# Kernel tuning notes

Measured on AMD Instinct MI355X. Metric: run time of the kernel, lower is better.

The kernel has to match this reference:

```python
import jax, jax.numpy as jnp
import numpy as np

EPS = 1e-5

def _lin_bn_relu(x, W, b, gamma, beta):
    # x: [N, Cin], W: [Cout, Cin] (torch layout), b/gamma/beta: [Cout]
    y = x @ W.T + b
    mu = jnp.mean(y, axis=0)                      # training-mode batch stats
    var = jnp.mean((y - mu) ** 2, axis=0)         # biased variance (torch BN)
    yhat = (y - mu) * jax.lax.rsqrt(var + EPS)
    return jax.nn.relu(gamma * yhat + beta)


def setup_inputs() -> dict:
    key = jax.random.key(0)
    ks = jax.random.split(key, 16)
    N = 262144
    dims = [(64, 3), (512, 64), (512, 512), (2, 512)]
    inp = {
        "x1": jax.random.normal(ks[0], (8, 4, 8, 8), dtype=jnp.float32),
        "x2": jax.random.normal(ks[1], (N, 3), dtype=jnp.float32),
    }
    for i, (co, ci) in enumerate(dims, start=1):
        lim = 1.0 / np.sqrt(ci)
        inp[f"W{i}"] = jax.random.uniform(ks[2 * i], (co, ci), jnp.float32, -lim, lim)
        inp[f"b{i}"] = jax.random.uniform(ks[2 * i + 1], (co,), jnp.float32, -lim, lim)
    for i, c in enumerate([64, 512, 512], start=1):
        inp[f"gamma{i}"] = jnp.ones((c,), jnp.float32)
        inp[f"beta{i}"] = jnp.zeros((c,), jnp.float32)
    return inp


def reference(x1, x2, W1, b1, W2, b2, W3, b3, W4, b4,
              gamma1, beta1, gamma2, beta2, gamma3, beta3):
    # x1 is sliced in the original forward (x[0][:, 0:-1]) but unused in the output.
    h = _lin_bn_relu(x2, W1, b1, gamma1, beta1)   # [N, 64]
    h = _lin_bn_relu(h, W2, b2, gamma2, beta2)    # [N, 512]
    h = _lin_bn_relu(h, W3, b3, gamma3, beta3)    # [N, 512]
    out = h @ W4.T + b4                           # [N, 2]
    return out
```

## Files before the change

kernel.cpp:

```cpp
#include <hip/hip_runtime.h>

typedef __bf16 bf16x4 __attribute__((ext_vector_type(4)));
typedef __bf16 bf16x8 __attribute__((ext_vector_type(8)));
typedef float f32x4 __attribute__((ext_vector_type(4)));

#define MFMA_BF16 __builtin_amdgcn_mfma_f32_16x16x32_bf16

__global__ __launch_bounds__(256) void prep_stats1_kernel(
    const float* __restrict__ x, const float* __restrict__ W1,
    const float* __restrict__ b1, const float* __restrict__ W2,
    const float* __restrict__ W3, __bf16* __restrict__ W2bf,
    __bf16* __restrict__ W3bf, float* __restrict__ gsum,
    float* __restrict__ gsq) {
  const int b = blockIdx.x;
  const int t = threadIdx.x;
  if (b >= 2048) {
    const float* src;
    __bf16* dst;
    int idx;
    if (b < 2064) {
      idx = (b - 2048) * 2048 + t * 8;
      src = W2;
      dst = W2bf;
    } else {
      idx = (b - 2064) * 2048 + t * 8;
      src = W3;
      dst = W3bf;
    }
    float4 f0 = *(const float4*)(src + idx);
    float4 f1 = *(const float4*)(src + idx + 4);
    bf16x8 o;
    o[0] = (__bf16)f0.x;
    o[1] = (__bf16)f0.y;
    o[2] = (__bf16)f0.z;
    o[3] = (__bf16)f0.w;
    o[4] = (__bf16)f1.x;
    o[5] = (__bf16)f1.y;
    o[6] = (__bf16)f1.z;
    o[7] = (__bf16)f1.w;
    *(bf16x8*)(dst + idx) = o;
    return;
  }
  int c = t & 63;
  int rw = t >> 6;
  float w0 = W1[c * 3 + 0], w1 = W1[c * 3 + 1], w2 = W1[c * 3 + 2];
  float bb = b1[c];
  int base = b * 128;
  float sum = 0.f, sq = 0.f;
#pragma unroll 4
  for (int i = 0; i < 32; ++i) {
    int row = base + i * 4 + rw;
    const float* xp = x + (size_t)row * 3;
    float y = fmaf(xp[0], w0, fmaf(xp[1], w1, fmaf(xp[2], w2, bb)));
    sum += y;
    sq += y * y;
  }
  __shared__ float ssum[256], ssq[256];
  ssum[t] = sum;
  ssq[t] = sq;
  __syncthreads();
  if (t < 64) {
    float s = ssum[t] + ssum[t + 64] + ssum[t + 128] + ssum[t + 192];
    float q = ssq[t] + ssq[t + 64] + ssq[t + 128] + ssq[t + 192];
    atomicAdd(&gsum[t], s);
    atomicAdd(&gsq[t], q);
  }
}

__global__ __launch_bounds__(256, 4) void m1_kernel(
    const float* __restrict__ x2, const float* __restrict__ gsum1,
    const float* __restrict__ gsq1, const float* __restrict__ gamma1,
    const float* __restrict__ beta1, const float* __restrict__ W1,
    const float* __restrict__ b1, float* __restrict__ M1,
    float* __restrict__ s1, float invN) {
  __shared__ float sF[256];
  __shared__ float xs[768];
  __shared__ __bf16 h1T[64 * 264];
  __shared__ float s1s[4][64];

  const int t = threadIdx.x;
  const int lane = t & 63, wave = t >> 6;
  const int lrow = lane & 15, lgrp = lane >> 4;

  if (t < 64) {
    float mu = gsum1[t] * invN;
    float var = gsq1[t] * invN - mu * mu;
    float sc = gamma1[t] * rsqrtf(var + 1e-5f);
    float sh = beta1[t] - mu * sc;
    sF[t] = sc * W1[t * 3];
    sF[64 + t] = sc * W1[t * 3 + 1];
    sF[128 + t] = sc * W1[t * 3 + 2];
    sF[192 + t] = sc * b1[t] + sh;
  }
  if (t < 192)
    ((float4*)xs)[t] = ((const float4*)(x2 + (size_t)blockIdx.x * 768))[t];
  __syncthreads();

  const int c0 = (t & 3) * 16;
  const int r0 = t >> 2;
  float sAcc[16] = {};
#pragma unroll
  for (int s = 0; s < 4; ++s) {
    int r = r0 + s * 64;
    float X0 = xs[r * 3], X1 = xs[r * 3 + 1], X2 = xs[r * 3 + 2];
#pragma unroll
    for (int j = 0; j < 16; ++j) {
      int c = c0 + j;
      float h = fmaxf(
          fmaf(sF[c], X0, fmaf(sF[64 + c], X1, fmaf(sF[128 + c], X2, sF[192 + c]))),
          0.f);
      sAcc[j] += h;
      h1T[c * 264 + r] = (__bf16)h;
    }
  }
  __syncthreads();

  f32x4 acc[4] = {};
#pragma unroll
  for (int kk = 0; kk < 256; kk += 32) {
    bf16x8 af = *(const bf16x8*)&h1T[(wave * 16 + lrow) * 264 + kk + lgrp * 8];
#pragma unroll
    for (int n = 0; n < 4; ++n) {
      bf16x8 bfr = *(const bf16x8*)&h1T[(n * 16 + lrow) * 264 + kk + lgrp * 8];
      acc[n] = MFMA_BF16(af, bfr, acc[n], 0, 0, 0);
    }
  }
#pragma unroll
  for (int n = 0; n < 4; ++n)
#pragma unroll
    for (int rr = 0; rr < 4; ++rr)
      atomicAdd(&M1[(wave * 16 + lgrp * 4 + rr) * 64 + n * 16 + lrow],
                acc[n][rr]);

#pragma unroll
  for (int j = 0; j < 16; ++j) {
    float v = sAcc[j];
    v += __shfl_xor(v, 4);
    v += __shfl_xor(v, 8);
    v += __shfl_xor(v, 16);
    v += __shfl_xor(v, 32);
    if (lane < 4) s1s[wave][(lane & 3) * 16 + j] = v;
  }
  __syncthreads();
  if (t < 64)
    atomicAdd(&s1[t], s1s[0][t] + s1s[1][t] + s1s[2][t] + s1s[3][t]);
}

__global__ __launch_bounds__(256) void finalize2v_kernel(
    const float* __restrict__ M1, const float* __restrict__ s1,
    const float* __restrict__ W2, const float* __restrict__ b2,
    const float* __restrict__ gamma2, const float* __restrict__ beta2,
    float* __restrict__ scale2, float* __restrict__ shift2f, float fN) {
  __shared__ float sM[64 * 65];
  __shared__ float ss[64];
  int t = threadIdx.x;
  for (int i = t; i < 4096; i += 256) sM[(i >> 6) * 65 + (i & 63)] = M1[i];
  if (t < 64) ss[t] = s1[t];
  __syncthreads();
  int lane = t & 63;
  int col = blockIdx.x * 4 + (t >> 6);
  float wi = W2[(size_t)col * 64 + lane];
  float p = 0.f;
#pragma unroll
  for (int j = 0; j < 64; ++j) p = fmaf(sM[lane * 65 + j], __shfl(wi, j), p);
  float qi = wi * p;
  float swi = ss[lane] * wi;
#pragma unroll
  for (int off = 1; off < 64; off <<= 1) {
    qi += __shfl_xor(qi, off);
    swi += __shfl_xor(swi, off);
  }
  if (lane == 0) {
    float b = b2[col];
    float sy = swi + fN * b;
    float sqs = qi + 2.f * b * swi + fN * b * b;
    float mu = sy / fN;
    float var = sqs / fN - mu * mu;
    float sc = gamma2[col] * rsqrtf(var + 1e-5f);
    scale2[col] = sc;
    shift2f[col] = (beta2[col] - mu * sc) + sc * b;
  }
}

#define G3_LD(BUF, K)                                                        \
  _Pragma("unroll") for (int m = 0; m < 4; ++m) BUF[m] =                     \
      *(const bf16x8*)&h2r[(m * 16 + lrow) * 520 + (K) * 32 + lgrp * 8];

#define G3_MM(BUF, K)                                                        \
  __builtin_amdgcn_s_setprio(1);                                             \
  _Pragma("unroll") for (int m = 0; m < 4; ++m) {                            \
    acc[m][0] = MFMA_BF16(BUF[m], b3r[K][0], acc[m][0], 0, 0, 0);            \
    acc[m][1] = MFMA_BF16(BUF[m], b3r[K][1], acc[m][1], 0, 0, 0);            \
  }                                                                          \
  __builtin_amdgcn_s_setprio(0);

template <int MODE>
__global__ __launch_bounds__(512, 2) void fused_kernel(
    const float* __restrict__ x2, const float* __restrict__ gsum1,
    const float* __restrict__ gsq1, const float* __restrict__ gamma1,
    const float* __restrict__ beta1, const float* __restrict__ W1,
    const float* __restrict__ b1, const __bf16* __restrict__ W2bf,
    const float* __restrict__ scale2, const float* __restrict__ shift2f,
    const __bf16* __restrict__ W3bf, const float* __restrict__ b3,
    const float* __restrict__ gamma3, const float* __restrict__ beta3,
    const float* __restrict__ W4, const float* __restrict__ b4,
    float* __restrict__ gsum3, float* __restrict__ gsq3,
    float* __restrict__ out, __bf16* __restrict__ y3o, int gBase, int gCount,
    int rStoreRgs, float invN) {
  __shared__ __bf16 h1buf[2][64 * 72];
  __shared__ __bf16 h2buf[2][64 * 520];
  __shared__ float sF[256];
  __shared__ float sSc2[512], sSh2[512];
  __shared__ float outaccW[8][64][2];

  const int t = threadIdx.x;
  const int lane = t & 63, wave = t >> 6;
  const int lrow = lane & 15, lgrp = lane >> 4;
  const int colHalf = blockIdx.x & 1;
  const int rgFirst = gBase + (int)(blockIdx.x >> 1) * gCount;
  const int wCol3 = colHalf * 256 + wave * 32;
  const int wCol2 = wave * 64;
  const bool doStore = (MODE == 3) && (rgFirst < rStoreRgs);

  if (t < 64) {
    float mu = gsum1[t] * invN;
    float var = gsq1[t] * invN - mu * mu;
    float sc = gamma1[t] * rsqrtf(var + 1e-5f);
    float sh = beta1[t] - mu * sc;
    sF[t] = sc * W1[t * 3];
    sF[64 + t] = sc * W1[t * 3 + 1];
    sF[128 + t] = sc * W1[t * 3 + 2];
    sF[192 + t] = sc * b1[t] + sh;
  }
  sSc2[t] = scale2[t & 511];
  sSh2[t] = shift2f[t & 511];

  bf16x8 b2r[2][4];
#pragma unroll
  for (int kk = 0; kk < 2; ++kk)
#pragma unroll
    for (int n = 0; n < 4; ++n)
      b2r[kk][n] = *(const bf16x8*)&W2bf[(wCol2 + n * 16 + lrow) * 64 +
                                         kk * 32 + lgrp * 8];
  bf16x8 b3r[16][2];
#pragma unroll
  for (int k = 0; k < 16; ++k)
#pragma unroll
    for (int n = 0; n < 2; ++n)
      b3r[k][n] = *(const bf16x8*)&W3bf[(size_t)(wCol3 + n * 16 + lrow) * 512 +
                                        k * 32 + lgrp * 8];

  const int c3a = wCol3 + lrow, c3b = wCol3 + 16 + lrow;
  float b3a = 0.f, b3b = 0.f;
  float sc3a = 0.f, sc3b = 0.f, sh3a = 0.f, sh3b = 0.f;
  float w40a = 0.f, w40b = 0.f, w41a = 0.f, w41b = 0.f, B40 = 0.f, B41 = 0.f;
  if (MODE != 2) {
    b3a = b3[c3a];
    b3b = b3[c3b];
  } else {
    float mu = gsum3[c3a] * invN;
    float var = gsq3[c3a] * invN - mu * mu;
    sc3a = gamma3[c3a] * rsqrtf(var + 1e-5f);
    sh3a = sc3a * b3[c3a] + (beta3[c3a] - mu * sc3a);
    mu = gsum3[c3b] * invN;
    var = gsq3[c3b] * invN - mu * mu;
    sc3b = gamma3[c3b] * rsqrtf(var + 1e-5f);
    sh3b = sc3b * b3[c3b] + (beta3[c3b] - mu * sc3b);
    w40a = W4[c3a];
    w40b = W4[c3b];
    w41a = W4[512 + c3a];
    w41b = W4[512 + c3b];
    B40 = b4[0];
    B41 = b4[1];
  }
  float csA = 0.f, cqA = 0.f, csB = 0.f, cqB = 0.f;

  const int hr = t >> 3, hc0 = (t & 7) * 8;
  const float* xbase = x2 + ((size_t)rgFirst * 64 + hr) * 3;
  float xa, xb, xc;

  auto stageH1 = [&](__bf16* h1p) {
    bf16x8 hv;
#pragma unroll
    for (int j = 0; j < 8; ++j) {
      int c = hc0 + j;
      float h = fmaf(sF[c], xa,
                     fmaf(sF[64 + c], xb, fmaf(sF[128 + c], xc, sF[192 + c])));
      hv[j] = (__bf16)fmaxf(h, 0.f);
    }
    *(bf16x8*)&h1p[hr * 72 + hc0] = hv;
  };

  auto gemm2 = [&](const __bf16* h1p, __bf16* h2p) {
#pragma unroll
    for (int nh = 0; nh < 2; ++nh) {
      f32x4 a2[2][4] = {};
#pragma unroll
      for (int kk = 0; kk < 2; ++kk) {
        bf16x8 af0 = *(const bf16x8*)&h1p[(0 * 16 + lrow) * 72 + kk * 32 + lgrp * 8];
        bf16x8 af1 = *(const bf16x8*)&h1p[(1 * 16 + lrow) * 72 + kk * 32 + lgrp * 8];
        bf16x8 af2 = *(const bf16x8*)&h1p[(2 * 16 + lrow) * 72 + kk * 32 + lgrp * 8];
        bf16x8 af3 = *(const bf16x8*)&h1p[(3 * 16 + lrow) * 72 + kk * 32 + lgrp * 8];
#pragma unroll
        for (int n2 = 0; n2 < 2; ++n2) {
          int n = nh * 2 + n2;
          a2[n2][0] = MFMA_BF16(b2r[kk][n], af0, a2[n2][0], 0, 0, 0);
          a2[n2][1] = MFMA_BF16(b2r[kk][n], af1, a2[n2][1], 0, 0, 0);
          a2[n2][2] = MFMA_BF16(b2r[kk][n], af2, a2[n2][2], 0, 0, 0);
          a2[n2][3] = MFMA_BF16(b2r[kk][n], af3, a2[n2][3], 0, 0, 0);
        }
      }
#pragma unroll
      for (int n2 = 0; n2 < 2; ++n2) {
        int ch0 = wCol2 + (nh * 2 + n2) * 16 + lgrp * 4;
        float s0 = sSc2[ch0], s1v = sSc2[ch0 + 1], s2v = sSc2[ch0 + 2],
              s3v = sSc2[ch0 + 3];
        float z0 = sSh2[ch0], z1 = sSh2[ch0 + 1], z2 = sSh2[ch0 + 2],
              z3 = sSh2[ch0 + 3];
#pragma unroll
        for (int m = 0; m < 4; ++m) {
          int row = m * 16 + lrow;
          bf16x4 hv;
          hv[0] = (__bf16)fmaxf(fmaf(s0, a2[n2][m][0], z0), 0.f);
          hv[1] = (__bf16)fmaxf(fmaf(s1v, a2[n2][m][1], z1), 0.f);
          hv[2] = (__bf16)fmaxf(fmaf(s2v, a2[n2][m][2], z2), 0.f);
          hv[3] = (__bf16)fmaxf(fmaf(s3v, a2[n2][m][3], z3), 0.f);
          *(bf16x4*)&h2p[row * 520 + ch0] = hv;
        }
      }
    }
  };

  __syncthreads();

  xa = xbase[0];
  xb = xbase[1];
  xc = xbase[2];
  stageH1(h1buf[0]);
  __syncthreads();
  gemm2(h1buf[0], h2buf[0]);
  if (gCount > 1) {
    const float* xn = xbase + 192;
    xa = xn[0];
    xb = xn[1];
    xc = xn[2];
    stageH1(h1buf[1]);
  }
  __syncthreads();

  for (int g = 0; g < gCount; ++g) {
    const int rBase = (rgFirst + g) * 64;
    const __bf16* h2r = h2buf[g & 1];

    if (g + 2 < gCount) {
      const float* xn = xbase + (size_t)(g + 2) * 192;
      xa = xn[0];
      xb = xn[1];
      xc = xn[2];
    }

    if (g + 1 < gCount) gemm2(h1buf[(g + 1) & 1], h2buf[(g + 1) & 1]);
    if (g + 2 < gCount) stageH1(h1buf[g & 1]);

    f32x4 acc[4][2] = {};
    bf16x8 afA[4], afB[4];
    G3_LD(afA, 0)
#pragma unroll
    for (int k = 0; k < 16; k += 2) {
      G3_LD(afB, k + 1)
      G3_MM(afA, k)
      if (k < 14) { G3_LD(afA, k + 2) }
      G3_MM(afB, k + 1)
    }

    if (MODE != 2) {
#pragma unroll
      for (int m = 0; m < 4; ++m)
#pragma unroll
        for (int rr = 0; rr < 4; ++rr) {
          float ya = acc[m][0][rr] + b3a;
          float yb = acc[m][1][rr] + b3b;
          csA += ya;
          cqA = fmaf(ya, ya, cqA);
          csB += yb;
          cqB = fmaf(yb, yb, cqB);
          if (doStore) {
            size_t row = (size_t)(rBase + m * 16 + lgrp * 4 + rr);
            y3o[row * 512 + c3a] = (__bf16)ya;
            y3o[row * 512 + c3b] = (__bf16)yb;
          }
        }
    } else {
#pragma unroll
      for (int m = 0; m < 4; ++m)
#pragma unroll
        for (int rr = 0; rr < 4; ++rr) {
          float ha = fmaxf(fmaf(sc3a, acc[m][0][rr], sh3a), 0.f);
          float hb = fmaxf(fmaf(sc3b, acc[m][1][rr], sh3b), 0.f);
          float dd0 = fmaf(ha, w40a, hb * w40b);
          float dd1 = fmaf(ha, w41a, hb * w41b);
          dd0 += __shfl_xor(dd0, 1);
          dd1 += __shfl_xor(dd1, 1);
          dd0 += __shfl_xor(dd0, 2);
          dd1 += __shfl_xor(dd1, 2);
          dd0 += __shfl_xor(dd0, 4);
          dd1 += __shfl_xor(dd1, 4);
          dd0 += __shfl_xor(dd0, 8);
          dd1 += __shfl_xor(dd1, 8);
          if (lrow == 0) {
            int row = m * 16 + lgrp * 4 + rr;
            outaccW[wave][row][0] = dd0;
            outaccW[wave][row][1] = dd1;
          }
        }
    }
    __syncthreads();
  }

  if (MODE != 2) {
    csA += __shfl_xor(csA, 16);
    cqA += __shfl_xor(cqA, 16);
    csB += __shfl_xor(csB, 16);
    cqB += __shfl_xor(cqB, 16);
    csA += __shfl_xor(csA, 32);
    cqA += __shfl_xor(cqA, 32);
    csB += __shfl_xor(csB, 32);
    cqB += __shfl_xor(cqB, 32);
    if (lgrp == 0) {
      atomicAdd(&gsum3[c3a], csA);
      atomicAdd(&gsq3[c3a], cqA);
      atomicAdd(&gsum3[c3b], csB);
      atomicAdd(&gsq3[c3b], cqB);
    }
  } else {
    if (t < 128) {
      int row = t >> 1, o = t & 1;
      float s = 0.f;
#pragma unroll
      for (int w = 0; w < 8; ++w) s += outaccW[w][row][o];
      if (colHalf == 0) s += (o == 0) ? B40 : B41;
      atomicAdd(&out[(size_t)(rgFirst * 64 + row) * 2 + o], s);
    }
  }
}

__global__ __launch_bounds__(256) void stream_out_kernel(
    const __bf16* __restrict__ y3, const float* __restrict__ gsum3,
    const float* __restrict__ gsq3, const float* __restrict__ gamma3,
    const float* __restrict__ beta3, const float* __restrict__ W4,
    const float* __restrict__ b4, float* __restrict__ out, int N, float invN) {
  __shared__ float sSc[512], sSh[512], sW0[512], sW1[512];
  int t = threadIdx.x;
  for (int i = t; i < 512; i += 256) {
    float mu = gsum3[i] * invN;
    float var = gsq3[i] * invN - mu * mu;
    float sc = gamma3[i] * rsqrtf(var + 1e-5f);
    sSc[i] = sc;
    sSh[i] = beta3[i] - mu * sc;
    sW0[i] = W4[i];
    sW1[i] = W4[512 + i];
  }
  __syncthreads();
  int lane = t & 63, wv = t >> 6;
  int c0 = lane * 8;
  float fsc[8], fsh[8], fw0[8], fw1[8];
#pragma unroll
  for (int j = 0; j < 8; ++j) {
    fsc[j] = sSc[c0 + j];
    fsh[j] = sSh[c0 + j];
    fw0[j] = sW0[c0 + j];
    fw1[j] = sW1[c0 + j];
  }
  float B0 = b4[0], B1 = b4[1];
  for (size_t row = (size_t)blockIdx.x * 8 + wv * 2; row < (size_t)N;
       row += (size_t)gridDim.x * 8) {
    bf16x8 v0 = *(const bf16x8*)(y3 + row * 512 + c0);
    bf16x8 v1 = *(const bf16x8*)(y3 + (row + 1) * 512 + c0);
    float d0a = 0.f, d1a = 0.f, d0b = 0.f, d1b = 0.f;
#pragma unroll
    for (int j = 0; j < 8; ++j) {
      float ha = fmaxf(fmaf(fsc[j], (float)v0[j], fsh[j]), 0.f);
      float hb = fmaxf(fmaf(fsc[j], (float)v1[j], fsh[j]), 0.f);
      d0a = fmaf(ha, fw0[j], d0a);
      d1a = fmaf(ha, fw1[j], d1a);
      d0b = fmaf(hb, fw0[j], d0b);
      d1b = fmaf(hb, fw1[j], d1b);
    }
    float t0 = d0a + __shfl_xor(d0a, 1);
    float t1 = d1a + __shfl_xor(d1a, 1);
    float t2 = d0b + __shfl_xor(d0b, 1);
    float t3 = d1b + __shfl_xor(d1b, 1);
    float u0 = (lane & 1) ? t1 : t0;
    float u1 = (lane & 1) ? t3 : t2;
    u0 += __shfl_xor(u0, 2);
    u1 += __shfl_xor(u1, 2);
    float w = (lane & 2) ? u1 : u0;
    w += __shfl_xor(w, 4);
    w += __shfl_xor(w, 8);
    w += __shfl_xor(w, 16);
    w += __shfl_xor(w, 32);
    if (lane < 4) out[row * 2 + lane] = w + ((lane & 1) ? B1 : B0);
  }
}

extern "C" void kernel_launch(void* const* d_in, const int* in_sizes, int n_in,
                              void* d_out, int out_size, void* d_ws,
                              size_t ws_size, hipStream_t stream) {
  const float* x2 = (const float*)d_in[1];
  const float* W1 = (const float*)d_in[2];
  const float* b1 = (const float*)d_in[3];
  const float* W2 = (const float*)d_in[4];
  const float* b2 = (const float*)d_in[5];
  const float* W3 = (const float*)d_in[6];
  const float* b3 = (const float*)d_in[7];
  const float* W4 = (const float*)d_in[8];
  const float* b4 = (const float*)d_in[9];
  const float* gamma1 = (const float*)d_in[10];
  const float* beta1 = (const float*)d_in[11];
  const float* gamma2 = (const float*)d_in[12];
  const float* beta2 = (const float*)d_in[13];
  const float* gamma3 = (const float*)d_in[14];
  const float* beta3 = (const float*)d_in[15];
  float* out = (float*)d_out;

  const int N = in_sizes[1] / 3;
  const float invN = 1.0f / (float)N;

  float* f0 = (float*)d_ws;
  float* gsum1 = f0;
  float* gsq1 = f0 + 64;
  float* M1 = f0 + 128;
  float* s1 = f0 + 4224;
  float* gsum3 = f0 + 4288;
  float* gsq3 = f0 + 4800;
  float* scale2 = f0 + 5312;
  float* shift2f = f0 + 5824;
  __bf16* W2bf = (__bf16*)(f0 + 6336);
  __bf16* W3bf = W2bf + 32768;

  const size_t y3off = (size_t)1 << 20;
  size_t availRows = (ws_size > y3off) ? (ws_size - y3off) / 1024 : 0;
  int rStoreBlks = (int)((availRows / 1024 < (size_t)(N / 1024))
                             ? availRows / 1024
                             : (size_t)(N / 1024));
  const int rStore = rStoreBlks * 1024;
  __bf16* y3bf = (__bf16*)((char*)d_ws + y3off);

  hipMemsetAsync(f0, 0, 5312 * sizeof(float), stream);
  prep_stats1_kernel<<<2192, 256, 0, stream>>>(x2, W1, b1, W2, W3, W2bf, W3bf,
                                               gsum1, gsq1);
  m1_kernel<<<N / 256, 256, 0, stream>>>(x2, gsum1, gsq1, gamma1, beta1, W1,
                                         b1, M1, s1, invN);
  finalize2v_kernel<<<128, 256, 0, stream>>>(M1, s1, W2, b2, gamma2, beta2,
                                             scale2, shift2f, (float)N);

  fused_kernel<3><<<(N / 1024) * 2, 512, 0, stream>>>(
      x2, gsum1, gsq1, gamma1, beta1, W1, b1, W2bf, scale2, shift2f, W3bf, b3,
      gamma3, beta3, W4, b4, gsum3, gsq3, out, y3bf, 0, 16, rStoreBlks * 16,
      invN);

  if (rStore > 0)
    stream_out_kernel<<<2048, 256, 0, stream>>>(y3bf, gsum3, gsq3, gamma3,
                                                beta3, W4, b4, out, rStore,
                                                invN);
  if (rStore < N) {
    hipMemsetAsync(out + (size_t)rStore * 2, 0,
                   (size_t)(N - rStore) * 2 * sizeof(float), stream);
    fused_kernel<2><<<((N - rStore) / 64) * 2, 512, 0, stream>>>(
        x2, gsum1, gsq1, gamma1, beta1, W1, b1, W2bf, scale2, shift2f, W3bf,
        b3, gamma3, beta3, W4, b4, gsum3, gsq3, out, y3bf, rStore / 64, 1, 0,
        invN);
  }
}
```

Before: 384.1 us.

## Derive BN1 stats from input moments; stagger gemm2/gemm3 order across waves

Replaces the per-channel layer-1 sum and sum-of-squares pass with a reduction of the nine first- and second-order moments of the 3-wide input. BN1 mean and variance are then computed analytically from W1 and b1 inside each consumer kernel. This cuts the stats kernel from 2048 blocks to 64 and reduces global atomics to 9 per block. Separately, in the fused kernel, half the waves run gemm3 before gemm2/stageH1 while the other half run it after, so MFMA and LDS phases interleave across waves. The moment formula in fp32 over 262k rows may lose some precision in the variance.

New measurement: 403.1 us. 1.05x slower.

```diff
diff --git a/kernel.cpp b/kernel.cpp
--- a/kernel.cpp
+++ b/kernel.cpp
@@ -6,24 +6,22 @@
 
 #define MFMA_BF16 __builtin_amdgcn_mfma_f32_16x16x32_bf16
 
-__global__ __launch_bounds__(256) void prep_stats1_kernel(
-    const float* __restrict__ x, const float* __restrict__ W1,
-    const float* __restrict__ b1, const float* __restrict__ W2,
+__global__ __launch_bounds__(256) void prep_xmom_kernel(
+    const float* __restrict__ x, const float* __restrict__ W2,
     const float* __restrict__ W3, __bf16* __restrict__ W2bf,
-    __bf16* __restrict__ W3bf, float* __restrict__ gsum,
-    float* __restrict__ gsq) {
+    __bf16* __restrict__ W3bf, float* __restrict__ xmom) {
   const int b = blockIdx.x;
   const int t = threadIdx.x;
-  if (b >= 2048) {
+  if (b >= 64) {
     const float* src;
     __bf16* dst;
     int idx;
-    if (b < 2064) {
-      idx = (b - 2048) * 2048 + t * 8;
+    if (b < 80) {
+      idx = (b - 64) * 2048 + t * 8;
       src = W2;
       dst = W2bf;
     } else {
-      idx = (b - 2064) * 2048 + t * 8;
+      idx = (b - 80) * 2048 + t * 8;
       src = W3;
       dst = W3bf;
     }
@@ -41,38 +39,68 @@
     *(bf16x8*)(dst + idx) = o;
     return;
   }
-  int c = t & 63;
-  int rw = t >> 6;
-  float w0 = W1[c * 3 + 0], w1 = W1[c * 3 + 1], w2 = W1[c * 3 + 2];
-  float bb = b1[c];
-  int base = b * 128;
-  float sum = 0.f, sq = 0.f;
+  float m[9] = {};
 #pragma unroll 4
-  for (int i = 0; i < 32; ++i) {
-    int row = base + i * 4 + rw;
-    const float* xp = x + (size_t)row * 3;
-    float y = fmaf(xp[0], w0, fmaf(xp[1], w1, fmaf(xp[2], w2, bb)));
-    sum += y;
-    sq += y * y;
-  }
-  __shared__ float ssum[256], ssq[256];
-  ssum[t] = sum;
-  ssq[t] = sq;
-  __syncthreads();
-  if (t < 64) {
-    float s = ssum[t] + ssum[t + 64] + ssum[t + 128] + ssum[t + 192];
-    float q = ssq[t] + ssq[t + 64] + ssq[t + 128] + ssq[t + 192];
-    atomicAdd(&gsum[t], s);
-    atomicAdd(&gsq[t], q);
-  }
+  for (int i = 0; i < 16; ++i) {
+    int r = b * 4096 + i * 256 + t;
+    const float* xp = x + (size_t)r * 3;
+    float a = xp[0], bb = xp[1], c = xp[2];
+    m[0] += a;
+    m[1] += bb;
+    m[2] += c;
+    m[3] = fmaf(a, a, m[3]);
+    m[4] = fmaf(a, bb, m[4]);
+    m[5] = fmaf(a, c, m[5]);
+    m[6] = fmaf(bb, bb, m[6]);
+    m[7] = fmaf(bb, c, m[7]);
+    m[8] = fmaf(c, c, m[8]);
+  }
+  __shared__ float red[4][9];
+  int lane = t & 63, wave = t >> 6;
+#pragma unroll
+  for (int j = 0; j < 9; ++j) {
+    float v = m[j];
+    v += __shfl_xor(v, 1);
+    v += __shfl_xor(v, 2);
+    v += __shfl_xor(v, 4);
+    v += __shfl_xor(v, 8);
+    v += __shfl_xor(v, 16);
+    v += __shfl_xor(v, 32);
+    if (lane == 0) red[wave][j] = v;
+  }
+  __syncthreads();
+  if (t < 9) atomicAdd(&xmom[t], red[0][t] + red[1][t] + red[2][t] + red[3][t]);
 }
 
+__device__ __forceinline__ void bn1_fold(const float* __restrict__ xm,
+                                         const float* __restrict__ W1,
+                                         const float* __restrict__ b1,
+                                         const float* __restrict__ gamma1,
+                                         const float* __restrict__ beta1,
+                                         int c, float invN, float fN,
+                                         float* f0, float* f1, float* f2,
+                                         float* f3) {
+  float w0 = W1[c * 3], w1 = W1[c * 3 + 1], w2 = W1[c * 3 + 2], bb = b1[c];
+  float wx = w0 * xm[0] + w1 * xm[1] + w2 * xm[2];
+  float sy = wx + fN * bb;
+  float q = w0 * w0 * xm[3] + 2.f * w0 * w1 * xm[4] + 2.f * w0 * w2 * xm[5] +
+            w1 * w1 * xm[6] + 2.f * w1 * w2 * xm[7] + w2 * w2 * xm[8] +
+            2.f * bb * wx + fN * bb * bb;
+  float mu = sy * invN;
+  float var = q * invN - mu * mu;
+  float sc = gamma1[c] * rsqrtf(var + 1e-5f);
+  float sh = beta1[c] - mu * sc;
+  *f0 = sc * w0;
+  *f1 = sc * w1;
+  *f2 = sc * w2;
+  *f3 = sc * bb + sh;
+}
+
 __global__ __launch_bounds__(256, 4) void m1_kernel(
-    const float* __restrict__ x2, const float* __restrict__ gsum1,
-    const float* __restrict__ gsq1, const float* __restrict__ gamma1,
-    const float* __restrict__ beta1, const float* __restrict__ W1,
-    const float* __restrict__ b1, float* __restrict__ M1,
-    float* __restrict__ s1, float invN) {
+    const float* __restrict__ x2, const float* __restrict__ xmom,
+    const float* __restrict__ gamma1, const float* __restrict__ beta1,
+    const float* __restrict__ W1, const float* __restrict__ b1,
+    float* __restrict__ M1, float* __restrict__ s1, float invN, float fN) {
   __shared__ float sF[256];
   __shared__ float xs[768];
   __shared__ __bf16 h1T[64 * 264];
@@ -83,14 +111,12 @@
   const int lrow = lane & 15, lgrp = lane >> 4;
 
   if (t < 64) {
-    float mu = gsum1[t] * invN;
-    float var = gsq1[t] * invN - mu * mu;
-    float sc = gamma1[t] * rsqrtf(var + 1e-5f);
-    float sh = beta1[t] - mu * sc;
-    sF[t] = sc * W1[t * 3];
-    sF[64 + t] = sc * W1[t * 3 + 1];
-    sF[128 + t] = sc * W1[t * 3 + 2];
-    sF[192 + t] = sc * b1[t] + sh;
+    float f0, f1, f2, f3;
+    bn1_fold(xmom, W1, b1, gamma1, beta1, t, invN, fN, &f0, &f1, &f2, &f3);
+    sF[t] = f0;
+    sF[64 + t] = f1;
+    sF[128 + t] = f2;
+    sF[192 + t] = f3;
   }
   if (t < 192)
     ((float4*)xs)[t] = ((const float4*)(x2 + (size_t)blockIdx.x * 768))[t];
@@ -196,17 +222,17 @@
 
 template <int MODE>
 __global__ __launch_bounds__(512, 2) void fused_kernel(
-    const float* __restrict__ x2, const float* __restrict__ gsum1,
-    const float* __restrict__ gsq1, const float* __restrict__ gamma1,
-    const float* __restrict__ beta1, const float* __restrict__ W1,
-    const float* __restrict__ b1, const __bf16* __restrict__ W2bf,
-    const float* __restrict__ scale2, const float* __restrict__ shift2f,
-    const __bf16* __restrict__ W3bf, const float* __restrict__ b3,
-    const float* __restrict__ gamma3, const float* __restrict__ beta3,
-    const float* __restrict__ W4, const float* __restrict__ b4,
-    float* __restrict__ gsum3, float* __restrict__ gsq3,
-    float* __restrict__ out, __bf16* __restrict__ y3o, int gBase, int gCount,
-    int rStoreRgs, float invN) {
+    const float* __restrict__ x2, const float* __restrict__ xmom,
+    const float* __restrict__ gamma1, const float* __restrict__ beta1,
+    const float* __restrict__ W1, const float* __restrict__ b1,
+    const __bf16* __restrict__ W2bf, const float* __restrict__ scale2,
+    const float* __restrict__ shift2f, const __bf16* __restrict__ W3bf,
+    const float* __restrict__ b3, const float* __restrict__ gamma3,
+    const float* __restrict__ beta3, const float* __restrict__ W4,
+    const float* __restrict__ b4, float* __restrict__ gsum3,
+    float* __restrict__ gsq3, float* __restrict__ out,
+    __bf16* __restrict__ y3o, int gBase, int gCount, int rStoreRgs,
+    float invN, float fN) {
   __shared__ __bf16 h1buf[2][64 * 72];
   __shared__ __bf16 h2buf[2][64 * 520];
   __shared__ float sF[256];
@@ -223,14 +249,12 @@
   const bool doStore = (MODE == 3) && (rgFirst < rStoreRgs);
 
   if (t < 64) {
-    float mu = gsum1[t] * invN;
-    float var = gsq1[t] * invN - mu * mu;
-    float sc = gamma1[t] * rsqrtf(var + 1e-5f);
-    float sh = beta1[t] - mu * sc;
-    sF[t] = sc * W1[t * 3];
-    sF[64 + t] = sc * W1[t * 3 + 1];
-    sF[128 + t] = sc * W1[t * 3 + 2];
-    sF[192 + t] = sc * b1[t] + sh;
+    float f0, f1, f2, f3;
+    bn1_fold(xmom, W1, b1, gamma1, beta1, t, invN, fN, &f0, &f1, &f2, &f3);
+    sF[t] = f0;
+    sF[64 + t] = f1;
+    sF[128 + t] = f2;
+    sF[192 + t] = f3;
   }
   sSc2[t] = scale2[t & 511];
   sSh2[t] = shift2f[t & 511];
@@ -359,18 +383,31 @@
       xc = xn[2];
     }
 
-    if (g + 1 < gCount) gemm2(h1buf[(g + 1) & 1], h2buf[(g + 1) & 1]);
-    if (g + 2 < gCount) stageH1(h1buf[g & 1]);
-
-    f32x4 acc[4][2] = {};
-    bf16x8 afA[4], afB[4];
-    G3_LD(afA, 0)
-#pragma unroll
-    for (int k = 0; k < 16; k += 2) {
-      G3_LD(afB, k + 1)
-      G3_MM(afA, k)
-      if (k < 14) { G3_LD(afA, k + 2) }
-      G3_MM(afB, k + 1)
+    f32x4 acc[4][2];
+    auto gemm3 = [&]() {
+#pragma unroll
+      for (int m = 0; m < 4; ++m)
+#pragma unroll
+        for (int n = 0; n < 2; ++n) acc[m][n] = (f32x4){0.f, 0.f, 0.f, 0.f};
+      bf16x8 afA[4], afB[4];
+      G3_LD(afA, 0)
+#pragma unroll
+      for (int k = 0; k < 16; k += 2) {
+        G3_LD(afB, k + 1)
+        G3_MM(afA, k)
+        if (k < 14) { G3_LD(afA, k + 2) }
+        G3_MM(afB, k + 1)
+      }
+    };
+
+    if (wave < 4) {
+      if (g + 1 < gCount) gemm2(h1buf[(g + 1) & 1], h2buf[(g + 1) & 1]);
+      if (g + 2 < gCount) stageH1(h1buf[g & 1]);
+      gemm3();
+    } else {
+      gemm3();
+      if (g + 1 < gCount) gemm2(h1buf[(g + 1) & 1], h2buf[(g + 1) & 1]);
+      if (g + 2 < gCount) stageH1(h1buf[g & 1]);
     }
 
     if (MODE != 2) {
@@ -525,17 +562,17 @@
 
   const int N = in_sizes[1] / 3;
   const float invN = 1.0f / (float)N;
+  const float fN = (float)N;
 
   float* f0 = (float*)d_ws;
-  float* gsum1 = f0;
-  float* gsq1 = f0 + 64;
-  float* M1 = f0 + 128;
-  float* s1 = f0 + 4224;
-  float* gsum3 = f0 + 4288;
-  float* gsq3 = f0 + 4800;
-  float* scale2 = f0 + 5312;
-  float* shift2f = f0 + 5824;
-  __bf16* W2bf = (__bf16*)(f0 + 6336);
+  float* xmom = f0;
+  float* M1 = f0 + 16;
+  float* s1 = f0 + 4112;
+  float* gsum3 = f0 + 4176;
+  float* gsq3 = f0 + 4688;
+  float* scale2 = f0 + 5200;
+  float* shift2f = f0 + 5712;
+  __bf16* W2bf = (__bf16*)(f0 + 6224);
   __bf16* W3bf = W2bf + 32768;
 
   const size_t y3off = (size_t)1 << 20;
@@ -546,18 +583,17 @@
   const int rStore = rStoreBlks * 1024;
   __bf16* y3bf = (__bf16*)((char*)d_ws + y3off);
 
-  hipMemsetAsync(f0, 0, 5312 * sizeof(float), stream);
-  prep_stats1_kernel<<<2192, 256, 0, stream>>>(x2, W1, b1, W2, W3, W2bf, W3bf,
-                                               gsum1, gsq1);
-  m1_kernel<<<N / 256, 256, 0, stream>>>(x2, gsum1, gsq1, gamma1, beta1, W1,
-                                         b1, M1, s1, invN);
+  hipMemsetAsync(f0, 0, 5200 * sizeof(float), stream);
+  prep_xmom_kernel<<<208, 256, 0, stream>>>(x2, W2, W3, W2bf, W3bf, xmom);
+  m1_kernel<<<N / 256, 256, 0, stream>>>(x2, xmom, gamma1, beta1, W1, b1, M1,
+                                         s1, invN, fN);
   finalize2v_kernel<<<128, 256, 0, stream>>>(M1, s1, W2, b2, gamma2, beta2,
-                                             scale2, shift2f, (float)N);
+                                             scale2, shift2f, fN);
 
   fused_kernel<3><<<(N / 1024) * 2, 512, 0, stream>>>(
-      x2, gsum1, gsq1, gamma1, beta1, W1, b1, W2bf, scale2, shift2f, W3bf, b3,
+      x2, xmom, gamma1, beta1, W1, b1, W2bf, scale2, shift2f, W3bf, b3,
       gamma3, beta3, W4, b4, gsum3, gsq3, out, y3bf, 0, 16, rStoreBlks * 16,
-      invN);
+      invN, fN);
 
   if (rStore > 0)
     stream_out_kernel<<<2048, 256, 0, stream>>>(y3bf, gsum3, gsq3, gamma3,
@@ -567,8 +603,8 @@
     hipMemsetAsync(out + (size_t)rStore * 2, 0,
                    (size_t)(N - rStore) * 2 * sizeof(float), stream);
     fused_kernel<2><<<((N - rStore) / 64) * 2, 512, 0, stream>>>(
-        x2, gsum1, gsq1, gamma1, beta1, W1, b1, W2bf, scale2, shift2f, W3bf,
-        b3, gamma3, beta3, W4, b4, gsum3, gsq3, out, y3bf, rStore / 64, 1, 0,
-        invN);
+        x2, xmom, gamma1, beta1, W1, b1, W2bf, scale2, shift2f, W3bf, b3,
+        gamma3, beta3, W4, b4, gsum3, gsq3, out, y3bf, rStore / 64, 1, 0,
+        invN, fN);
   }
 }
```
